# Kernel tuning notes

Measured on AMD Instinct MI355X. Metric: run time of the kernel, lower is better.

Reference implementation:

```python
import jax, jax.numpy as jnp
import numpy as np

B, N, D = 8192, 1024, 3


def setup_inputs() -> dict:
    key = jax.random.key(0)
    k1, k2, k3, k4 = jax.random.split(key, 4)
    return {
        "x": jax.random.normal(k1, (B, N, D), dtype=jnp.float32),
        "mu_x": jax.random.normal(k2, (B, D), dtype=jnp.float32),
        "y": jax.random.normal(k3, (B, N, D), dtype=jnp.float32),
        "mu_y": jax.random.normal(k4, (B, D), dtype=jnp.float32),
    }


def reference(x, mu_x, y, mu_y):
    # Center both point clouds: [B, N, 3]
    xc = x - mu_x[:, None, :]
    yc = y - mu_y[:, None, :]
    # Cross-covariance per batch: [B, 3, 3]
    cov = jnp.einsum('bnd,bne->bde', xc, yc)
    # Batched 3x3 SVD; square matrices so full_matrices=False matches torch
    U, S, Vt = jnp.linalg.svd(cov, full_matrices=False)
    R = jnp.matmul(U, Vt)  # [B, 3, 3] (no det sign correction, as in source)
    # Frobenius norm over (points, dims) per batch
    xn = jnp.sqrt(jnp.sum(xc * xc, axis=(1, 2)))
    yn = jnp.sqrt(jnp.sum(yc * yc, axis=(1, 2)))
    scale_factor_S = yn / (xn + 1e-6)  # [B]
    # Translation: t = mu_y - R @ mu_x
    t = mu_y - jnp.einsum('bij,bj->bi', R, mu_x)  # [B, 3]
    return (R, t, scale_factor_S)
```

## Files before the change

kernel.cpp:

```cpp
#include <hip/hip_runtime.h>

#define NB 8192
#define NPTS 1024

__global__ __launch_bounds__(256) void fused_kernel(
    const float* __restrict__ x, const float* __restrict__ y,
    const float* __restrict__ mu_x, const float* __restrict__ mu_y,
    float* __restrict__ out)
{
    __shared__ float4 sx[768];
    __shared__ float4 sy[768];
    __shared__ float red[4][12];

    const int t = threadIdx.x;
    const int b = blockIdx.x;

    const float4* x4 = (const float4*)(x + (size_t)b * (NPTS * 3));
    const float4* y4 = (const float4*)(y + (size_t)b * (NPTS * 3));

    const float4 a0 = x4[t], a1 = x4[t + 256], a2 = x4[t + 512];
    const float4 c0 = y4[t], c1 = y4[t + 256], c2 = y4[t + 512];

    const float mx0 = mu_x[b * 3 + 0], mx1 = mu_x[b * 3 + 1], mx2 = mu_x[b * 3 + 2];
    const float my0 = mu_y[b * 3 + 0], my1 = mu_y[b * 3 + 1], my2 = mu_y[b * 3 + 2];

    sx[t] = a0; sx[t + 256] = a1; sx[t + 512] = a2;
    sy[t] = c0; sy[t + 256] = c1; sy[t + 512] = c2;
    __syncthreads();

    const float4 xa = sx[3 * t + 0], xb4 = sx[3 * t + 1], xc4 = sx[3 * t + 2];
    const float4 ya = sy[3 * t + 0], yb4 = sy[3 * t + 1], yc4 = sy[3 * t + 2];

    const float xp[4][3] = {{xa.x, xa.y, xa.z}, {xa.w, xb4.x, xb4.y},
                            {xb4.z, xb4.w, xc4.x}, {xc4.y, xc4.z, xc4.w}};
    const float yp[4][3] = {{ya.x, ya.y, ya.z}, {ya.w, yb4.x, yb4.y},
                            {yb4.z, yb4.w, yc4.x}, {yc4.y, yc4.z, yc4.w}};

    float v[11];
    #pragma unroll
    for (int i = 0; i < 11; ++i) v[i] = 0.0f;

    #pragma unroll
    for (int k = 0; k < 4; ++k) {
        const float xd0 = xp[k][0] - mx0, xd1 = xp[k][1] - mx1, xd2 = xp[k][2] - mx2;
        const float yd0 = yp[k][0] - my0, yd1 = yp[k][1] - my1, yd2 = yp[k][2] - my2;
        v[0] += xd0 * yd0; v[1] += xd0 * yd1; v[2] += xd0 * yd2;
        v[3] += xd1 * yd0; v[4] += xd1 * yd1; v[5] += xd1 * yd2;
        v[6] += xd2 * yd0; v[7] += xd2 * yd1; v[8] += xd2 * yd2;
        v[9]  += xd0 * xd0 + xd1 * xd1 + xd2 * xd2;
        v[10] += yd0 * yd0 + yd1 * yd1 + yd2 * yd2;
    }

    #pragma unroll
    for (int off = 32; off >= 1; off >>= 1) {
        #pragma unroll
        for (int i = 0; i < 11; ++i) v[i] += __shfl_xor(v[i], off, 64);
    }

    if ((t & 63) == 0) {
        #pragma unroll
        for (int i = 0; i < 11; ++i) red[t >> 6][i] = v[i];
    }
    __syncthreads();

    if (t < 64) {
        float s[11];
        #pragma unroll
        for (int i = 0; i < 11; ++i)
            s[i] = red[0][i] + red[1][i] + red[2][i] + red[3][i];

        float Q[9] = {s[0], s[1], s[2], s[3], s[4], s[5], s[6], s[7], s[8]};
        const float nxx = s[9];
        const float nyy = s[10];

        #pragma unroll
        for (int it = 0; it < 11; ++it) {
            float C[9];
            C[0] = Q[4] * Q[8] - Q[5] * Q[7];
            C[1] = Q[5] * Q[6] - Q[3] * Q[8];
            C[2] = Q[3] * Q[7] - Q[4] * Q[6];
            C[3] = Q[2] * Q[7] - Q[1] * Q[8];
            C[4] = Q[0] * Q[8] - Q[2] * Q[6];
            C[5] = Q[1] * Q[6] - Q[0] * Q[7];
            C[6] = Q[1] * Q[5] - Q[2] * Q[4];
            C[7] = Q[2] * Q[3] - Q[0] * Q[5];
            C[8] = Q[0] * Q[4] - Q[1] * Q[3];
            const float det = Q[0] * C[0] + Q[1] * C[1] + Q[2] * C[2];
            const float invdet = __builtin_amdgcn_rcpf(det);

            float nq = 0.0f, nc = 0.0f;
            #pragma unroll
            for (int i = 0; i < 9; ++i) { nq += Q[i] * Q[i]; nc += C[i] * C[i]; }
            const float g  = __builtin_amdgcn_sqrtf(__builtin_amdgcn_sqrtf(
                                 nc * invdet * invdet * __builtin_amdgcn_rcpf(nq)));
            const float hg = 0.5f * g;
            const float hi = 0.5f * invdet * __builtin_amdgcn_rcpf(g);
            #pragma unroll
            for (int i = 0; i < 9; ++i) Q[i] = hg * Q[i] + hi * C[i];
        }

        if (t == 0) {
            #pragma unroll
            for (int i = 0; i < 9; ++i) out[(size_t)b * 9 + i] = Q[i];

            float* tout = out + (size_t)NB * 9 + (size_t)b * 3;
            tout[0] = my0 - (Q[0] * mx0 + Q[1] * mx1 + Q[2] * mx2);
            tout[1] = my1 - (Q[3] * mx0 + Q[4] * mx1 + Q[5] * mx2);
            tout[2] = my2 - (Q[6] * mx0 + Q[7] * mx1 + Q[8] * mx2);

            out[(size_t)NB * 12 + b] =
                __builtin_amdgcn_sqrtf(nyy) / (__builtin_amdgcn_sqrtf(nxx) + 1e-6f);
        }
    }
}

extern "C" void kernel_launch(void* const* d_in, const int* in_sizes, int n_in,
                              void* d_out, int out_size, void* d_ws, size_t ws_size,
                              hipStream_t stream) {
    const float* x    = (const float*)d_in[0];
    const float* mu_x = (const float*)d_in[1];
    const float* y    = (const float*)d_in[2];
    const float* mu_y = (const float*)d_in[3];
    float* out = (float*)d_out;
    (void)d_ws; (void)ws_size;

    fused_kernel<<<dim3(NB), dim3(256), 0, stream>>>(x, y, mu_x, mu_y, out);
}
```

Before: 221.4 us.

## Assign two batches per wavefront with register double-buffered loads, no LDS

Each 64-lane wavefront now processes two batches in eight chunks of 256 points. It prefetches the next chunk into a second register buffer while it computes the current one. This removes the shared-memory staging, the block barriers and the cross-wave reduction, and cuts the grid to 2048 blocks of 128 threads. The cost is that each lane reads three contiguous float4s per chunk (strided access per lane, less coalesced), there is less parallelism per batch, and the serial SVD iteration now runs twice per wave.

```diff
diff --git a/kernel.cpp b/kernel.cpp
--- a/kernel.cpp
+++ b/kernel.cpp
@@ -2,114 +2,127 @@
 
 #define NB 8192
 #define NPTS 1024
+#define NBLK 2048
+#define TPB 128
 
-__global__ __launch_bounds__(256) void fused_kernel(
+__global__ __launch_bounds__(TPB) void fused_kernel(
     const float* __restrict__ x, const float* __restrict__ y,
     const float* __restrict__ mu_x, const float* __restrict__ mu_y,
     float* __restrict__ out)
 {
-    __shared__ float4 sx[768];
-    __shared__ float4 sy[768];
-    __shared__ float red[4][12];
+    const int lane = threadIdx.x & 63;
+    const int wid  = blockIdx.x * (TPB / 64) + (threadIdx.x >> 6);
+    const int b0   = wid * 2;
 
-    const int t = threadIdx.x;
-    const int b = blockIdx.x;
+    float4 bx[2][3], by[2][3];
 
-    const float4* x4 = (const float4*)(x + (size_t)b * (NPTS * 3));
-    const float4* y4 = (const float4*)(y + (size_t)b * (NPTS * 3));
+    float mx0 = mu_x[b0 * 3 + 0], mx1 = mu_x[b0 * 3 + 1], mx2 = mu_x[b0 * 3 + 2];
+    float my0 = mu_y[b0 * 3 + 0], my1 = mu_y[b0 * 3 + 1], my2 = mu_y[b0 * 3 + 2];
 
-    const float4 a0 = x4[t], a1 = x4[t + 256], a2 = x4[t + 512];
-    const float4 c0 = y4[t], c1 = y4[t + 256], c2 = y4[t + 512];
-
-    const float mx0 = mu_x[b * 3 + 0], mx1 = mu_x[b * 3 + 1], mx2 = mu_x[b * 3 + 2];
-    const float my0 = mu_y[b * 3 + 0], my1 = mu_y[b * 3 + 1], my2 = mu_y[b * 3 + 2];
-
-    sx[t] = a0; sx[t + 256] = a1; sx[t + 512] = a2;
-    sy[t] = c0; sy[t + 256] = c1; sy[t + 512] = c2;
-    __syncthreads();
-
-    const float4 xa = sx[3 * t + 0], xb4 = sx[3 * t + 1], xc4 = sx[3 * t + 2];
-    const float4 ya = sy[3 * t + 0], yb4 = sy[3 * t + 1], yc4 = sy[3 * t + 2];
-
-    const float xp[4][3] = {{xa.x, xa.y, xa.z}, {xa.w, xb4.x, xb4.y},
-                            {xb4.z, xb4.w, xc4.x}, {xc4.y, xc4.z, xc4.w}};
-    const float yp[4][3] = {{ya.x, ya.y, ya.z}, {ya.w, yb4.x, yb4.y},
-                            {yb4.z, yb4.w, yc4.x}, {yc4.y, yc4.z, yc4.w}};
+    {
+        const float4* x4 = (const float4*)(x + (size_t)b0 * (NPTS * 3));
+        const float4* y4 = (const float4*)(y + (size_t)b0 * (NPTS * 3));
+        const int base = 3 * lane;
+        bx[0][0] = x4[base + 0]; bx[0][1] = x4[base + 1]; bx[0][2] = x4[base + 2];
+        by[0][0] = y4[base + 0]; by[0][1] = y4[base + 1]; by[0][2] = y4[base + 2];
+    }
 
     float v[11];
     #pragma unroll
     for (int i = 0; i < 11; ++i) v[i] = 0.0f;
 
     #pragma unroll
-    for (int k = 0; k < 4; ++k) {
-        const float xd0 = xp[k][0] - mx0, xd1 = xp[k][1] - mx1, xd2 = xp[k][2] - mx2;
-        const float yd0 = yp[k][0] - my0, yd1 = yp[k][1] - my1, yd2 = yp[k][2] - my2;
-        v[0] += xd0 * yd0; v[1] += xd0 * yd1; v[2] += xd0 * yd2;
-        v[3] += xd1 * yd0; v[4] += xd1 * yd1; v[5] += xd1 * yd2;
-        v[6] += xd2 * yd0; v[7] += xd2 * yd1; v[8] += xd2 * yd2;
-        v[9]  += xd0 * xd0 + xd1 * xd1 + xd2 * xd2;
-        v[10] += yd0 * yd0 + yd1 * yd1 + yd2 * yd2;
-    }
+    for (int s = 0; s < 8; ++s) {
+        if (s < 7) {
+            const int b = b0 + ((s + 1) >> 2);
+            const int c = (s + 1) & 3;
+            const float4* x4 = (const float4*)(x + (size_t)b * (NPTS * 3));
+            const float4* y4 = (const float4*)(y + (size_t)b * (NPTS * 3));
+            const int base = 3 * (c * 64 + lane);
+            const int sl = (s + 1) & 1;
+            bx[sl][0] = x4[base + 0]; bx[sl][1] = x4[base + 1]; bx[sl][2] = x4[base + 2];
+            by[sl][0] = y4[base + 0]; by[sl][1] = y4[base + 1]; by[sl][2] = y4[base + 2];
+        }
 
-    #pragma unroll
-    for (int off = 32; off >= 1; off >>= 1) {
-        #pragma unroll
-        for (int i = 0; i < 11; ++i) v[i] += __shfl_xor(v[i], off, 64);
-    }
+        const int sl = s & 1;
+        const float4 xa = bx[sl][0], xb4 = bx[sl][1], xc4 = bx[sl][2];
+        const float4 ya = by[sl][0], yb4 = by[sl][1], yc4 = by[sl][2];
 
-    if ((t & 63) == 0) {
-        #pragma unroll
-        for (int i = 0; i < 11; ++i) red[t >> 6][i] = v[i];
-    }
-    __syncthreads();
-
-    if (t < 64) {
-        float s[11];
-        #pragma unroll
-        for (int i = 0; i < 11; ++i)
-            s[i] = red[0][i] + red[1][i] + red[2][i] + red[3][i];
-
-        float Q[9] = {s[0], s[1], s[2], s[3], s[4], s[5], s[6], s[7], s[8]};
-        const float nxx = s[9];
-        const float nyy = s[10];
+        const float xp[4][3] = {{xa.x, xa.y, xa.z}, {xa.w, xb4.x, xb4.y},
+                                {xb4.z, xb4.w, xc4.x}, {xc4.y, xc4.z, xc4.w}};
+        const float yp[4][3] = {{ya.x, ya.y, ya.z}, {ya.w, yb4.x, yb4.y},
+                                {yb4.z, yb4.w, yc4.x}, {yc4.y, yc4.z, yc4.w}};
 
         #pragma unroll
-        for (int it = 0; it < 11; ++it) {
-            float C[9];
-            C[0] = Q[4] * Q[8] - Q[5] * Q[7];
-            C[1] = Q[5] * Q[6] - Q[3] * Q[8];
-            C[2] = Q[3] * Q[7] - Q[4] * Q[6];
-            C[3] = Q[2] * Q[7] - Q[1] * Q[8];
-            C[4] = Q[0] * Q[8] - Q[2] * Q[6];
-            C[5] = Q[1] * Q[6] - Q[0] * Q[7];
-            C[6] = Q[1] * Q[5] - Q[2] * Q[4];
-            C[7] = Q[2] * Q[3] - Q[0] * Q[5];
-            C[8] = Q[0] * Q[4] - Q[1] * Q[3];
-            const float det = Q[0] * C[0] + Q[1] * C[1] + Q[2] * C[2];
-            const float invdet = __builtin_amdgcn_rcpf(det);
-
-            float nq = 0.0f, nc = 0.0f;
-            #pragma unroll
-            for (int i = 0; i < 9; ++i) { nq += Q[i] * Q[i]; nc += C[i] * C[i]; }
-            const float g  = __builtin_amdgcn_sqrtf(__builtin_amdgcn_sqrtf(
-                                 nc * invdet * invdet * __builtin_amdgcn_rcpf(nq)));
-            const float hg = 0.5f * g;
-            const float hi = 0.5f * invdet * __builtin_amdgcn_rcpf(g);
-            #pragma unroll
-            for (int i = 0; i < 9; ++i) Q[i] = hg * Q[i] + hi * C[i];
+        for (int k = 0; k < 4; ++k) {
+            const float xd0 = xp[k][0] - mx0, xd1 = xp[k][1] - mx1, xd2 = xp[k][2] - mx2;
+            const float yd0 = yp[k][0] - my0, yd1 = yp[k][1] - my1, yd2 = yp[k][2] - my2;
+            v[0] += xd0 * yd0; v[1] += xd0 * yd1; v[2] += xd0 * yd2;
+            v[3] += xd1 * yd0; v[4] += xd1 * yd1; v[5] += xd1 * yd2;
+            v[6] += xd2 * yd0; v[7] += xd2 * yd1; v[8] += xd2 * yd2;
+            v[9]  += xd0 * xd0 + xd1 * xd1 + xd2 * xd2;
+            v[10] += yd0 * yd0 + yd1 * yd1 + yd2 * yd2;
         }
 
-        if (t == 0) {
+        if ((s & 3) == 3) {
+            const int b = b0 + (s >> 2);
+
             #pragma unroll
-            for (int i = 0; i < 9; ++i) out[(size_t)b * 9 + i] = Q[i];
+            for (int off = 32; off >= 1; off >>= 1) {
+                #pragma unroll
+                for (int i = 0; i < 11; ++i) v[i] += __shfl_xor(v[i], off, 64);
+            }
 
-            float* tout = out + (size_t)NB * 9 + (size_t)b * 3;
-            tout[0] = my0 - (Q[0] * mx0 + Q[1] * mx1 + Q[2] * mx2);
-            tout[1] = my1 - (Q[3] * mx0 + Q[4] * mx1 + Q[5] * mx2);
-            tout[2] = my2 - (Q[6] * mx0 + Q[7] * mx1 + Q[8] * mx2);
+            float Q[9] = {v[0], v[1], v[2], v[3], v[4], v[5], v[6], v[7], v[8]};
+            const float nxx = v[9];
+            const float nyy = v[10];
 
-            out[(size_t)NB * 12 + b] =
-                __builtin_amdgcn_sqrtf(nyy) / (__builtin_amdgcn_sqrtf(nxx) + 1e-6f);
+            #pragma unroll
+            for (int it = 0; it < 11; ++it) {
+                float C[9];
+                C[0] = Q[4] * Q[8] - Q[5] * Q[7];
+                C[1] = Q[5] * Q[6] - Q[3] * Q[8];
+                C[2] = Q[3] * Q[7] - Q[4] * Q[6];
+                C[3] = Q[2] * Q[7] - Q[1] * Q[8];
+                C[4] = Q[0] * Q[8] - Q[2] * Q[6];
+                C[5] = Q[1] * Q[6] - Q[0] * Q[7];
+                C[6] = Q[1] * Q[5] - Q[2] * Q[4];
+                C[7] = Q[2] * Q[3] - Q[0] * Q[5];
+                C[8] = Q[0] * Q[4] - Q[1] * Q[3];
+                const float det = Q[0] * C[0] + Q[1] * C[1] + Q[2] * C[2];
+                const float invdet = __builtin_amdgcn_rcpf(det);
+
+                float nq = 0.0f, nc = 0.0f;
+                #pragma unroll
+                for (int i = 0; i < 9; ++i) { nq += Q[i] * Q[i]; nc += C[i] * C[i]; }
+                const float g  = __builtin_amdgcn_sqrtf(__builtin_amdgcn_sqrtf(
+                                     nc * invdet * invdet * __builtin_amdgcn_rcpf(nq)));
+                const float hg = 0.5f * g;
+                const float hi = 0.5f * invdet * __builtin_amdgcn_rcpf(g);
+                #pragma unroll
+                for (int i = 0; i < 9; ++i) Q[i] = hg * Q[i] + hi * C[i];
+            }
+
+            if (lane == 0) {
+                #pragma unroll
+                for (int i = 0; i < 9; ++i) out[(size_t)b * 9 + i] = Q[i];
+
+                float* tout = out + (size_t)NB * 9 + (size_t)b * 3;
+                tout[0] = my0 - (Q[0] * mx0 + Q[1] * mx1 + Q[2] * mx2);
+                tout[1] = my1 - (Q[3] * mx0 + Q[4] * mx1 + Q[5] * mx2);
+                tout[2] = my2 - (Q[6] * mx0 + Q[7] * mx1 + Q[8] * mx2);
+
+                out[(size_t)NB * 12 + b] =
+                    __builtin_amdgcn_sqrtf(nyy) / (__builtin_amdgcn_sqrtf(nxx) + 1e-6f);
+            }
+
+            #pragma unroll
+            for (int i = 0; i < 11; ++i) v[i] = 0.0f;
+            if (s < 7) {
+                const int bn = b + 1;
+                mx0 = mu_x[bn * 3 + 0]; mx1 = mu_x[bn * 3 + 1]; mx2 = mu_x[bn * 3 + 2];
+                my0 = mu_y[bn * 3 + 0]; my1 = mu_y[bn * 3 + 1]; my2 = mu_y[bn * 3 + 2];
+            }
         }
     }
 }
@@ -124,5 +137,5 @@
     float* out = (float*)d_out;
     (void)d_ws; (void)ws_size;
 
-    fused_kernel<<<dim3(NB), dim3(256), 0, stream>>>(x, y, mu_x, mu_y, out);
+    fused_kernel<<<dim3(NBLK), dim3(TPB), 0, stream>>>(x, y, mu_x, mu_y, out);
 }
```

Result: slower. 227.2 us (+2.6%).
